# Kernel optimization log

Hardware: AMD Instinct MI355X
Metric: run time of the kernel (lower is better)

Reference implementation:

```python
import jax, jax.numpy as jnp
import numpy as np

N_NODES = 100000


def setup_inputs() -> dict:
    key = jax.random.key(0)
    k_x, k_r, k_c, k_v, k_t = jax.random.split(key, 5)
    n_edges = 3200000
    fin, fout = 512, 128
    x = jax.random.normal(k_x, (N_NODES, fin), dtype=jnp.float32)
    rows = jax.random.randint(k_r, (n_edges,), 0, N_NODES, dtype=jnp.int32)
    cols = jax.random.randint(k_c, (n_edges,), 0, N_NODES, dtype=jnp.int32)
    vals = jax.random.uniform(k_v, (n_edges,), dtype=jnp.float32)
    theta = jax.random.normal(k_t, (fin, fout), dtype=jnp.float32) * (1.0 / np.sqrt(fin))
    bias = jnp.zeros((fout,), dtype=jnp.float32)
    return {"x": x, "rows": rows, "cols": cols, "vals": vals, "theta": theta, "bias": bias}


def reference(x, rows, cols, vals, theta, bias):
    # SpMM: mx[i] = sum over edges (i <- j) of A[i,j] * x[j]
    gathered = vals[:, None] * x[cols]                      # [E, fin]
    mx = jax.ops.segment_sum(gathered, rows, num_segments=N_NODES)  # [N, fin]
    # Dense feature transform + bias + relu
    o = jnp.einsum('nf,fo->no', mx, theta) + bias           # [N, fout]
    return jax.nn.relu(o)
```

## Files before the change

kernel.cpp:

```cpp
#include <hip/hip_runtime.h>
#include <stdint.h>
#include <stddef.h>

#define FIN 512
#define FOUT 128
#define BROWS 160
#define NBK 625
#define SORT_CAP 7680
#define TILE 8192
#define MAXNT 512

typedef __attribute__((ext_vector_type(8))) short short8;
typedef __attribute__((ext_vector_type(4))) float f32x4;

__device__ __forceinline__ unsigned short f2bf(float f) {
  unsigned u = __builtin_bit_cast(unsigned, f);
  u = (u + 0x7fffu + ((u >> 16) & 1u)) >> 16;
  return (unsigned short)u;
}
__device__ __forceinline__ float bf2f(unsigned short h) {
  unsigned u = ((unsigned)h) << 16;
  return __builtin_bit_cast(float, u);
}

__global__ void prep_theta_k(const float* __restrict__ theta,
                             unsigned short* __restrict__ thetaT) {
  int idx = blockIdx.x * blockDim.x + threadIdx.x;
  int n = idx >> 9;
  int k = idx & 511;
  thetaT[idx] = f2bf(theta[k * FOUT + n]);
}

__global__ __launch_bounds__(256) void gemm_k(const float* __restrict__ x,
                                              const unsigned short* __restrict__ thetaT,
                                              unsigned short* __restrict__ yb, int M) {
  __shared__ __align__(16) unsigned short lA[128 * 40];
  __shared__ __align__(16) unsigned short lB[128 * 40];
  const int tid = threadIdx.x;
  const int row0 = blockIdx.x * 128;
  const int wave = tid >> 6, lane = tid & 63;
  const int wm = wave >> 1, wn = wave & 1;
  const int fr = lane & 15, fq = lane >> 4;
  const int arow = tid >> 1, ahalf = tid & 1;

  f32x4 acc[4][4] = {};

  const int grow = row0 + arow;
  const bool aval = (grow < M);
  const float* asrc = x + (size_t)(aval ? grow : 0) * FIN + ahalf * 16;
  const unsigned short* bsrc = thetaT + (size_t)arow * FIN + ahalf * 16;

  for (int k0 = 0; k0 < FIN; k0 += 32) {
    float av[16];
    if (aval) {
      const float4* p = (const float4*)(asrc + k0);
      float4 v0 = p[0], v1 = p[1], v2 = p[2], v3 = p[3];
      av[0] = v0.x; av[1] = v0.y; av[2] = v0.z; av[3] = v0.w;
      av[4] = v1.x; av[5] = v1.y; av[6] = v1.z; av[7] = v1.w;
      av[8] = v2.x; av[9] = v2.y; av[10] = v2.z; av[11] = v2.w;
      av[12] = v3.x; av[13] = v3.y; av[14] = v3.z; av[15] = v3.w;
    } else {
      for (int i = 0; i < 16; i++) av[i] = 0.f;
    }
    unsigned ap[8];
    for (int i = 0; i < 8; i++)
      ap[i] = (unsigned)f2bf(av[2 * i]) | ((unsigned)f2bf(av[2 * i + 1]) << 16);
    uint4* aw = (uint4*)&lA[arow * 40 + ahalf * 16];
    aw[0] = make_uint4(ap[0], ap[1], ap[2], ap[3]);
    aw[1] = make_uint4(ap[4], ap[5], ap[6], ap[7]);

    const uint4* bp = (const uint4*)(bsrc + k0);
    uint4 b0 = bp[0], b1 = bp[1];
    uint4* bw = (uint4*)&lB[arow * 40 + ahalf * 16];
    bw[0] = b0; bw[1] = b1;

    __syncthreads();

    short8 af[4], bfv[4];
#pragma unroll
    for (int m = 0; m < 4; m++)
      af[m] = *(const short8*)&lA[(wm * 64 + m * 16 + fr) * 40 + fq * 8];
#pragma unroll
    for (int n = 0; n < 4; n++)
      bfv[n] = *(const short8*)&lB[(wn * 64 + n * 16 + fr) * 40 + fq * 8];
#pragma unroll
    for (int m = 0; m < 4; m++)
#pragma unroll
      for (int n = 0; n < 4; n++)
        acc[m][n] = __builtin_amdgcn_mfma_f32_16x16x32_bf16(af[m], bfv[n], acc[m][n], 0, 0, 0);

    __syncthreads();
  }

#pragma unroll
  for (int m = 0; m < 4; m++) {
    int rbase = row0 + wm * 64 + m * 16 + fq * 4;
#pragma unroll
    for (int j = 0; j < 4; j++) {
      int r = rbase + j;
      if (r < M) {
        unsigned short* dst = yb + (size_t)r * FOUT + wn * 64;
#pragma unroll
        for (int n = 0; n < 4; n++) dst[n * 16 + fr] = f2bf(acc[m][n][j]);
      }
    }
  }
}

__global__ __launch_bounds__(256) void tilesort_k(const int* __restrict__ rows,
                                                  const int* __restrict__ cols,
                                                  const float* __restrict__ vals,
                                                  unsigned* __restrict__ rec4tile,
                                                  unsigned char* __restrict__ rlotile,
                                                  int* __restrict__ lofs,
                                                  int* __restrict__ btotals, int E) {
  __shared__ int hist[NBK];
  __shared__ int wsum[4];
  __shared__ unsigned srec[TILE];
  __shared__ unsigned char srlo[TILE];
  const int c = blockIdx.x, t = threadIdx.x;
  const int base = c * TILE;
  const int n = (E - base < TILE) ? (E - base) : TILE;

  for (int i = t; i < NBK; i += 256) hist[i] = 0;
  __syncthreads();

#pragma unroll
  for (int k = 0; k < TILE / 256; k++) {
    int i = base + k * 256 + t;
    if (i < E) atomicAdd(&hist[rows[i] / BROWS], 1);
  }
  __syncthreads();

  int c0 = t * 3, c1 = c0 + 1, c2 = c0 + 2;
  int h0 = (c0 < NBK) ? hist[c0] : 0;
  int h1 = (c1 < NBK) ? hist[c1] : 0;
  int h2 = (c2 < NBK) ? hist[c2] : 0;
  if (h0) atomicAdd(&btotals[c0], h0);
  if (h1) atomicAdd(&btotals[c1], h1);
  if (h2) atomicAdd(&btotals[c2], h2);
  int loc = h0 + h1 + h2;
  int lane = t & 63, wv = t >> 6;
  int inc = loc;
  for (int off = 1; off < 64; off <<= 1) {
    int u = __shfl_up(inc, off, 64);
    if (lane >= off) inc += u;
  }
  if (lane == 63) wsum[wv] = inc;
  __syncthreads();
  int excl = inc - loc;
  for (int i = 0; i < 4; i++)
    if (i < wv) excl += wsum[i];

  size_t lbase = (size_t)c * (NBK + 1);
  int e = excl;
  if (c0 <= NBK) lofs[lbase + c0] = e;
  __syncthreads();
  if (c0 < NBK) hist[c0] = e;
  e += h0;
  if (c1 <= NBK) lofs[lbase + c1] = e;
  if (c1 < NBK) hist[c1] = e;
  e += h1;
  if (c2 <= NBK) lofs[lbase + c2] = e;
  if (c2 < NBK) hist[c2] = e;
  __syncthreads();

#pragma unroll
  for (int k = 0; k < TILE / 256; k++) {
    int i = base + k * 256 + t;
    if (i < E) {
      int r = rows[i];
      int b = r / BROWS;
      int p = atomicAdd(&hist[b], 1);
      srec[p] = ((unsigned)cols[i] << 15) | ((unsigned)f2bf(vals[i]) & 0x7fffu);
      srlo[p] = (unsigned char)(r - b * BROWS);
    }
  }
  __syncthreads();

  for (int j = t; j < n; j += 256) {
    rec4tile[base + j] = srec[j];
    rlotile[base + j] = srlo[j];
  }
}

__global__ __launch_bounds__(1024) void bscan_k(const int* __restrict__ btotals,
                                                int* __restrict__ boff,
                                                int* __restrict__ offsets,
                                                int E, int M) {
  __shared__ int tmp[1024];
  int t = threadIdx.x;
  tmp[t] = (t < NBK) ? btotals[t] : 0;
  __syncthreads();
  for (int off = 1; off < 1024; off <<= 1) {
    int v = (t >= off) ? tmp[t - off] : 0;
    __syncthreads();
    tmp[t] += v;
    __syncthreads();
  }
  if (t < NBK) boff[t] = t ? tmp[t - 1] : 0;
  if (t == 0) {
    boff[NBK] = E;
    offsets[M] = E;
  }
}

__global__ __launch_bounds__(256) void bsort_k(const int* __restrict__ boff,
                                               const int* __restrict__ lofs,
                                               const unsigned* __restrict__ rec4tile,
                                               const unsigned char* __restrict__ rlotile,
                                               unsigned* __restrict__ rec4s,
                                               int* __restrict__ offsets,
                                               int NT, int M) {
  __shared__ unsigned s4[SORT_CAP];
  __shared__ unsigned char k8[SORT_CAP];
  __shared__ int lh[256];
  __shared__ int lsc[256];
  __shared__ int wsum[4];
  __shared__ int fsrc[MAXNT];
  __shared__ int fdst[MAXNT];
  __shared__ int flen[MAXNT];
  int b = blockIdx.x, t = threadIdx.x;
  int start = boff[b];

  int ca = 2 * t, cb = 2 * t + 1;
  int la = 0, fa = 0, lb2 = 0, fb = 0;
  if (ca < NT) {
    size_t p = (size_t)ca * (NBK + 1) + b;
    la = lofs[p];
    fa = lofs[p + 1] - la;
  }
  if (cb < NT) {
    size_t p = (size_t)cb * (NBK + 1) + b;
    lb2 = lofs[p];
    fb = lofs[p + 1] - lb2;
  }
  int loc = fa + fb;
  int lane = t & 63, wv = t >> 6;
  int inc = loc;
  for (int off = 1; off < 64; off <<= 1) {
    int u = __shfl_up(inc, off, 64);
    if (lane >= off) inc += u;
  }
  if (lane == 63) wsum[wv] = inc;
  __syncthreads();
  int excl = inc - loc;
  for (int i = 0; i < 4; i++)
    if (i < wv) excl += wsum[i];

  if (ca < NT) {
    fsrc[ca] = ca * TILE + la;
    fdst[ca] = excl;
    flen[ca] = fa;
  }
  if (cb < NT) {
    fsrc[cb] = cb * TILE + lb2;
    fdst[cb] = excl + fa;
    flen[cb] = fb;
  }
  lh[t] = 0;
  __syncthreads();

  int grp = t >> 4, l16 = t & 15;
  for (int f = grp; f < NT; f += 16) {
    int L = flen[f];
    int sd = fdst[f];
    int ss = fsrc[f];
    for (int j = l16; j < L; j += 16) {
      int d = sd + j;
      if (d < SORT_CAP) {
        s4[d] = rec4tile[ss + j];
        k8[d] = rlotile[ss + j];
      }
    }
  }

  int n = boff[b + 1] - start;
  if (n > SORT_CAP) n = SORT_CAP;
  __syncthreads();

  for (int i = t; i < n; i += 256) atomicAdd(&lh[k8[i]], 1);
  __syncthreads();
  lsc[t] = lh[t];
  __syncthreads();
  for (int off = 1; off < 256; off <<= 1) {
    int v = (t >= off) ? lsc[t - off] : 0;
    __syncthreads();
    lsc[t] += v;
    __syncthreads();
  }
  int ex = t ? lsc[t - 1] : 0;
  int row = b * BROWS + t;
  if (t < BROWS && row < M) offsets[row] = start + ex;
  lh[t] = ex;
  __syncthreads();
  for (int i = t; i < n; i += 256) {
    unsigned r = s4[i];
    int p = atomicAdd(&lh[k8[i]], 1);
    rec4s[start + p] = r;
  }
}

__global__ __launch_bounds__(256) void rowv2_k(const int* __restrict__ offsets,
                                               const unsigned* __restrict__ rec4,
                                               const unsigned short* __restrict__ yb,
                                               const float* __restrict__ bias,
                                               float* __restrict__ out, int M) {
  int gid = blockIdx.x * blockDim.x + threadIdx.x;
  int r = gid >> 4;
  int l = gid & 15;
  if (r >= M) return;
  int s = offsets[r], e = offsets[r + 1];
  const unsigned short* src = yb + l * 8;

  float a0 = 0.f, a1 = 0.f, a2 = 0.f, a3 = 0.f, a4 = 0.f, a5 = 0.f, a6 = 0.f, a7 = 0.f;
  float c0 = 0.f, c1 = 0.f, c2 = 0.f, c3 = 0.f, c4 = 0.f, c5 = 0.f, c6 = 0.f, c7 = 0.f;

  int i = s;
  for (; i + 2 <= e; i += 2) {
    unsigned q0 = rec4[i];
    unsigned q1 = rec4[i + 1];
    const uint4 u0 = *(const uint4*)(src + (size_t)(q0 >> 15) * FOUT);
    const uint4 u1 = *(const uint4*)(src + (size_t)(q1 >> 15) * FOUT);
    float v0 = __builtin_bit_cast(float, (q0 & 0x7fffu) << 16);
    float v1 = __builtin_bit_cast(float, (q1 & 0x7fffu) << 16);
    a0 += v0 * __builtin_bit_cast(float, u0.x << 16);
    a1 += v0 * __builtin_bit_cast(float, u0.x & 0xffff0000u);
    a2 += v0 * __builtin_bit_cast(float, u0.y << 16);
    a3 += v0 * __builtin_bit_cast(float, u0.y & 0xffff0000u);
    a4 += v0 * __builtin_bit_cast(float, u0.z << 16);
    a5 += v0 * __builtin_bit_cast(float, u0.z & 0xffff0000u);
    a6 += v0 * __builtin_bit_cast(float, u0.w << 16);
    a7 += v0 * __builtin_bit_cast(float, u0.w & 0xffff0000u);
    c0 += v1 * __builtin_bit_cast(float, u1.x << 16);
    c1 += v1 * __builtin_bit_cast(float, u1.x & 0xffff0000u);
    c2 += v1 * __builtin_bit_cast(float, u1.y << 16);
    c3 += v1 * __builtin_bit_cast(float, u1.y & 0xffff0000u);
    c4 += v1 * __builtin_bit_cast(float, u1.z << 16);
    c5 += v1 * __builtin_bit_cast(float, u1.z & 0xffff0000u);
    c6 += v1 * __builtin_bit_cast(float, u1.w << 16);
    c7 += v1 * __builtin_bit_cast(float, u1.w & 0xffff0000u);
  }
  if (i < e) {
    unsigned q0 = rec4[i];
    const uint4 u0 = *(const uint4*)(src + (size_t)(q0 >> 15) * FOUT);
    float v0 = __builtin_bit_cast(float, (q0 & 0x7fffu) << 16);
    a0 += v0 * __builtin_bit_cast(float, u0.x << 16);
    a1 += v0 * __builtin_bit_cast(float, u0.x & 0xffff0000u);
    a2 += v0 * __builtin_bit_cast(float, u0.y << 16);
    a3 += v0 * __builtin_bit_cast(float, u0.y & 0xffff0000u);
    a4 += v0 * __builtin_bit_cast(float, u0.z << 16);
    a5 += v0 * __builtin_bit_cast(float, u0.z & 0xffff0000u);
    a6 += v0 * __builtin_bit_cast(float, u0.w << 16);
    a7 += v0 * __builtin_bit_cast(float, u0.w & 0xffff0000u);
  }

  const float4 b0 = *(const float4*)(bias + l * 8);
  const float4 b1 = *(const float4*)(bias + l * 8 + 4);
  float* dst = out + (size_t)r * FOUT + l * 8;
  float4 o0, o1;
  o0.x = fmaxf(a0 + c0 + b0.x, 0.f);
  o0.y = fmaxf(a1 + c1 + b0.y, 0.f);
  o0.z = fmaxf(a2 + c2 + b0.z, 0.f);
  o0.w = fmaxf(a3 + c3 + b0.w, 0.f);
  o1.x = fmaxf(a4 + c4 + b1.x, 0.f);
  o1.y = fmaxf(a5 + c5 + b1.y, 0.f);
  o1.z = fmaxf(a6 + c6 + b1.z, 0.f);
  o1.w = fmaxf(a7 + c7 + b1.w, 0.f);
  *(float4*)(dst) = o0;
  *(float4*)(dst + 4) = o1;
}

extern "C" void kernel_launch(void* const* d_in, const int* in_sizes, int n_in,
                              void* d_out, int out_size, void* d_ws, size_t ws_size,
                              hipStream_t stream) {
  const float* x = (const float*)d_in[0];
  const int* rows = (const int*)d_in[1];
  const int* cols = (const int*)d_in[2];
  const float* vals = (const float*)d_in[3];
  const float* theta = (const float*)d_in[4];
  const float* bias = (const float*)d_in[5];
  float* out = (float*)d_out;
  const int M = in_sizes[0] / FIN;
  const int E = in_sizes[1];
  const int NT = (E + TILE - 1) / TILE;

  char* w = (char*)d_ws;
  auto alloc = [&](size_t bytes) {
    char* p = w;
    w += (bytes + 255) & ~(size_t)255;
    return p;
  };
  unsigned short* yb = (unsigned short*)alloc((size_t)M * FOUT * 2);
  unsigned short* thetaT = (unsigned short*)alloc((size_t)FIN * FOUT * 2);
  unsigned* rec4tile = (unsigned*)alloc((size_t)NT * TILE * 4);
  unsigned char* rlotile = (unsigned char*)alloc((size_t)NT * TILE);
  int* lofs = (int*)alloc((size_t)NT * (NBK + 1) * 4);
  int* btotals = (int*)alloc((size_t)NBK * 4);
  int* boff = (int*)alloc((size_t)(NBK + 1) * 4);
  int* offsets = (int*)alloc((size_t)(M + 1) * 4);
  unsigned* rec4s = (unsigned*)alloc((size_t)E * 4);

  hipMemsetAsync(btotals, 0, (size_t)NBK * 4, stream);
  prep_theta_k<<<(FIN * FOUT) / 256, 256, 0, stream>>>(theta, thetaT);
  gemm_k<<<(M + 127) / 128, 256, 0, stream>>>(x, thetaT, yb, M);
  tilesort_k<<<NT, 256, 0, stream>>>(rows, cols, vals, rec4tile, rlotile, lofs, btotals, E);
  bscan_k<<<1, 1024, 0, stream>>>(btotals, boff, offsets, E, M);
  bsort_k<<<NBK, 256, 0, stream>>>(boff, lofs, rec4tile, rlotile, rec4s, offsets, NT, M);
  rowv2_k<<<(M * 16 + 255) / 256, 256, 0, stream>>>(offsets, rec4s, yb, bias, out, M);
}
```

Measured before the change: 294.9 us.

## Split projected features into column planes with XCD-affine persistent gather

The GEMM output is stored as 8 column planes of 16 bf16 each instead of row-major rows. The gather kernel becomes persistent: each block reads its XCD id, works through planes starting from its own, and takes row tiles from per-plane atomic queues. It stages each tile's edge records in LDS. The aim is for each XCD's L2 to hold one small feature plane (about 3.2 MB), so random gathers hit cache. The cost is that every edge record is read 8 times, plus queue atomics and extra barriers.

```diff
diff --git a/kernel.cpp b/kernel.cpp
--- a/kernel.cpp
+++ b/kernel.cpp
@@ -9,6 +9,9 @@
 #define SORT_CAP 7680
 #define TILE 8192
 #define MAXNT 512
+#define NCH 8
+#define PTILE 128
+#define PSTCAP 5120
 
 typedef __attribute__((ext_vector_type(8))) short short8;
 typedef __attribute__((ext_vector_type(4))) float f32x4;
@@ -33,7 +36,7 @@
 
 __global__ __launch_bounds__(256) void gemm_k(const float* __restrict__ x,
                                               const unsigned short* __restrict__ thetaT,
-                                              unsigned short* __restrict__ yb, int M) {
+                                              unsigned short* __restrict__ ybc, int M) {
   __shared__ __align__(16) unsigned short lA[128 * 40];
   __shared__ __align__(16) unsigned short lB[128 * 40];
   const int tid = threadIdx.x;
@@ -99,9 +102,11 @@
     for (int j = 0; j < 4; j++) {
       int r = rbase + j;
       if (r < M) {
-        unsigned short* dst = yb + (size_t)r * FOUT + wn * 64;
-#pragma unroll
-        for (int n = 0; n < 4; n++) dst[n * 16 + fr] = f2bf(acc[m][n][j]);
+#pragma unroll
+        for (int n = 0; n < 4; n++) {
+          int c = wn * 4 + n;
+          ybc[((size_t)c * M + r) * 16 + fr] = f2bf(acc[m][n][j]);
+        }
       }
     }
   }
@@ -187,6 +192,7 @@
 __global__ __launch_bounds__(1024) void bscan_k(const int* __restrict__ btotals,
                                                 int* __restrict__ boff,
                                                 int* __restrict__ offsets,
+                                                int* __restrict__ q,
                                                 int E, int M) {
   __shared__ int tmp[1024];
   int t = threadIdx.x;
@@ -199,6 +205,7 @@
     __syncthreads();
   }
   if (t < NBK) boff[t] = t ? tmp[t - 1] : 0;
+  if (t < NCH) q[t] = 0;
   if (t == 0) {
     boff[NBK] = E;
     offsets[M] = E;
@@ -301,74 +308,130 @@
   }
 }
 
-__global__ __launch_bounds__(256) void rowv2_k(const int* __restrict__ offsets,
-                                               const unsigned* __restrict__ rec4,
-                                               const unsigned short* __restrict__ yb,
-                                               const float* __restrict__ bias,
-                                               float* __restrict__ out, int M) {
-  int gid = blockIdx.x * blockDim.x + threadIdx.x;
-  int r = gid >> 4;
-  int l = gid & 15;
-  if (r >= M) return;
-  int s = offsets[r], e = offsets[r + 1];
-  const unsigned short* src = yb + l * 8;
-
-  float a0 = 0.f, a1 = 0.f, a2 = 0.f, a3 = 0.f, a4 = 0.f, a5 = 0.f, a6 = 0.f, a7 = 0.f;
-  float c0 = 0.f, c1 = 0.f, c2 = 0.f, c3 = 0.f, c4 = 0.f, c5 = 0.f, c6 = 0.f, c7 = 0.f;
-
-  int i = s;
-  for (; i + 2 <= e; i += 2) {
-    unsigned q0 = rec4[i];
-    unsigned q1 = rec4[i + 1];
-    const uint4 u0 = *(const uint4*)(src + (size_t)(q0 >> 15) * FOUT);
-    const uint4 u1 = *(const uint4*)(src + (size_t)(q1 >> 15) * FOUT);
-    float v0 = __builtin_bit_cast(float, (q0 & 0x7fffu) << 16);
-    float v1 = __builtin_bit_cast(float, (q1 & 0x7fffu) << 16);
-    a0 += v0 * __builtin_bit_cast(float, u0.x << 16);
-    a1 += v0 * __builtin_bit_cast(float, u0.x & 0xffff0000u);
-    a2 += v0 * __builtin_bit_cast(float, u0.y << 16);
-    a3 += v0 * __builtin_bit_cast(float, u0.y & 0xffff0000u);
-    a4 += v0 * __builtin_bit_cast(float, u0.z << 16);
-    a5 += v0 * __builtin_bit_cast(float, u0.z & 0xffff0000u);
-    a6 += v0 * __builtin_bit_cast(float, u0.w << 16);
-    a7 += v0 * __builtin_bit_cast(float, u0.w & 0xffff0000u);
-    c0 += v1 * __builtin_bit_cast(float, u1.x << 16);
-    c1 += v1 * __builtin_bit_cast(float, u1.x & 0xffff0000u);
-    c2 += v1 * __builtin_bit_cast(float, u1.y << 16);
-    c3 += v1 * __builtin_bit_cast(float, u1.y & 0xffff0000u);
-    c4 += v1 * __builtin_bit_cast(float, u1.z << 16);
-    c5 += v1 * __builtin_bit_cast(float, u1.z & 0xffff0000u);
-    c6 += v1 * __builtin_bit_cast(float, u1.w << 16);
-    c7 += v1 * __builtin_bit_cast(float, u1.w & 0xffff0000u);
-  }
-  if (i < e) {
-    unsigned q0 = rec4[i];
-    const uint4 u0 = *(const uint4*)(src + (size_t)(q0 >> 15) * FOUT);
-    float v0 = __builtin_bit_cast(float, (q0 & 0x7fffu) << 16);
-    a0 += v0 * __builtin_bit_cast(float, u0.x << 16);
-    a1 += v0 * __builtin_bit_cast(float, u0.x & 0xffff0000u);
-    a2 += v0 * __builtin_bit_cast(float, u0.y << 16);
-    a3 += v0 * __builtin_bit_cast(float, u0.y & 0xffff0000u);
-    a4 += v0 * __builtin_bit_cast(float, u0.z << 16);
-    a5 += v0 * __builtin_bit_cast(float, u0.z & 0xffff0000u);
-    a6 += v0 * __builtin_bit_cast(float, u0.w << 16);
-    a7 += v0 * __builtin_bit_cast(float, u0.w & 0xffff0000u);
-  }
-
-  const float4 b0 = *(const float4*)(bias + l * 8);
-  const float4 b1 = *(const float4*)(bias + l * 8 + 4);
-  float* dst = out + (size_t)r * FOUT + l * 8;
-  float4 o0, o1;
-  o0.x = fmaxf(a0 + c0 + b0.x, 0.f);
-  o0.y = fmaxf(a1 + c1 + b0.y, 0.f);
-  o0.z = fmaxf(a2 + c2 + b0.z, 0.f);
-  o0.w = fmaxf(a3 + c3 + b0.w, 0.f);
-  o1.x = fmaxf(a4 + c4 + b1.x, 0.f);
-  o1.y = fmaxf(a5 + c5 + b1.y, 0.f);
-  o1.z = fmaxf(a6 + c6 + b1.z, 0.f);
-  o1.w = fmaxf(a7 + c7 + b1.w, 0.f);
-  *(float4*)(dst) = o0;
-  *(float4*)(dst + 4) = o1;
+__global__ __launch_bounds__(256) void rowp_k(const int* __restrict__ offsets,
+                                              const unsigned* __restrict__ rec4,
+                                              const unsigned short* __restrict__ ybc,
+                                              const float* __restrict__ bias,
+                                              float* __restrict__ out,
+                                              int* __restrict__ q, int M) {
+  __shared__ unsigned st[PSTCAP];
+  __shared__ int loff[PTILE + 1];
+  __shared__ int s_tile;
+  unsigned xcd = __builtin_amdgcn_s_getreg((31u << 11) | 20u) & 7u;
+  const int ntiles = (M + PTILE - 1) / PTILE;
+  const int t = threadIdx.x;
+  const int rg = t >> 1;
+  const int h = t & 1;
+
+#pragma unroll 1
+  for (int d = 0; d < NCH; d++) {
+    int p = (xcd + d) & 7;
+    const unsigned short* plane = ybc + (size_t)p * M * 16;
+    const float4 bb0 = *(const float4*)(bias + p * 16 + h * 8);
+    const float4 bb1 = *(const float4*)(bias + p * 16 + h * 8 + 4);
+
+#pragma unroll 1
+    while (true) {
+      if (t == 0) s_tile = atomicAdd(&q[p], 1);
+      __syncthreads();
+      int tile = s_tile;
+      __syncthreads();
+      if (tile >= ntiles) break;
+
+      int base = tile * PTILE;
+      if (t <= PTILE) {
+        int idx = base + t;
+        loff[t] = offsets[idx > M ? M : idx];
+      }
+      __syncthreads();
+      int s0 = loff[0];
+      int n = loff[PTILE] - s0;
+      bool fits = (n <= PSTCAP);
+      if (fits) {
+        for (int i = t; i < n; i += 256)
+          st[i] = __builtin_nontemporal_load(&rec4[s0 + i]);
+      }
+      __syncthreads();
+
+      int r = base + rg;
+      if (r < M) {
+        int i0 = loff[rg] - s0, i1 = loff[rg + 1] - s0;
+        float a0 = 0.f, a1 = 0.f, a2 = 0.f, a3 = 0.f;
+        float a4 = 0.f, a5 = 0.f, a6 = 0.f, a7 = 0.f;
+        float c0 = 0.f, c1 = 0.f, c2 = 0.f, c3 = 0.f;
+        float c4 = 0.f, c5 = 0.f, c6 = 0.f, c7 = 0.f;
+        const unsigned short* src = plane + h * 8;
+        if (fits) {
+          int i = i0;
+          for (; i + 2 <= i1; i += 2) {
+            unsigned q0 = st[i];
+            unsigned q1 = st[i + 1];
+            const uint4 u0 = *(const uint4*)(src + (size_t)(q0 >> 15) * 16);
+            const uint4 u1 = *(const uint4*)(src + (size_t)(q1 >> 15) * 16);
+            float v0 = __builtin_bit_cast(float, (q0 & 0x7fffu) << 16);
+            float v1 = __builtin_bit_cast(float, (q1 & 0x7fffu) << 16);
+            a0 += v0 * __builtin_bit_cast(float, u0.x << 16);
+            a1 += v0 * __builtin_bit_cast(float, u0.x & 0xffff0000u);
+            a2 += v0 * __builtin_bit_cast(float, u0.y << 16);
+            a3 += v0 * __builtin_bit_cast(float, u0.y & 0xffff0000u);
+            a4 += v0 * __builtin_bit_cast(float, u0.z << 16);
+            a5 += v0 * __builtin_bit_cast(float, u0.z & 0xffff0000u);
+            a6 += v0 * __builtin_bit_cast(float, u0.w << 16);
+            a7 += v0 * __builtin_bit_cast(float, u0.w & 0xffff0000u);
+            c0 += v1 * __builtin_bit_cast(float, u1.x << 16);
+            c1 += v1 * __builtin_bit_cast(float, u1.x & 0xffff0000u);
+            c2 += v1 * __builtin_bit_cast(float, u1.y << 16);
+            c3 += v1 * __builtin_bit_cast(float, u1.y & 0xffff0000u);
+            c4 += v1 * __builtin_bit_cast(float, u1.z << 16);
+            c5 += v1 * __builtin_bit_cast(float, u1.z & 0xffff0000u);
+            c6 += v1 * __builtin_bit_cast(float, u1.w << 16);
+            c7 += v1 * __builtin_bit_cast(float, u1.w & 0xffff0000u);
+          }
+          if (i < i1) {
+            unsigned q0 = st[i];
+            const uint4 u0 = *(const uint4*)(src + (size_t)(q0 >> 15) * 16);
+            float v0 = __builtin_bit_cast(float, (q0 & 0x7fffu) << 16);
+            a0 += v0 * __builtin_bit_cast(float, u0.x << 16);
+            a1 += v0 * __builtin_bit_cast(float, u0.x & 0xffff0000u);
+            a2 += v0 * __builtin_bit_cast(float, u0.y << 16);
+            a3 += v0 * __builtin_bit_cast(float, u0.y & 0xffff0000u);
+            a4 += v0 * __builtin_bit_cast(float, u0.z << 16);
+            a5 += v0 * __builtin_bit_cast(float, u0.z & 0xffff0000u);
+            a6 += v0 * __builtin_bit_cast(float, u0.w << 16);
+            a7 += v0 * __builtin_bit_cast(float, u0.w & 0xffff0000u);
+          }
+        } else {
+          for (int i = i0; i < i1; i++) {
+            unsigned q0 = rec4[s0 + i];
+            const uint4 u0 = *(const uint4*)(src + (size_t)(q0 >> 15) * 16);
+            float v0 = __builtin_bit_cast(float, (q0 & 0x7fffu) << 16);
+            a0 += v0 * __builtin_bit_cast(float, u0.x << 16);
+            a1 += v0 * __builtin_bit_cast(float, u0.x & 0xffff0000u);
+            a2 += v0 * __builtin_bit_cast(float, u0.y << 16);
+            a3 += v0 * __builtin_bit_cast(float, u0.y & 0xffff0000u);
+            a4 += v0 * __builtin_bit_cast(float, u0.z << 16);
+            a5 += v0 * __builtin_bit_cast(float, u0.z & 0xffff0000u);
+            a6 += v0 * __builtin_bit_cast(float, u0.w << 16);
+            a7 += v0 * __builtin_bit_cast(float, u0.w & 0xffff0000u);
+          }
+        }
+
+        float* dst = out + (size_t)r * FOUT + p * 16 + h * 8;
+        f32x4 o0, o1;
+        o0[0] = fmaxf(a0 + c0 + bb0.x, 0.f);
+        o0[1] = fmaxf(a1 + c1 + bb0.y, 0.f);
+        o0[2] = fmaxf(a2 + c2 + bb0.z, 0.f);
+        o0[3] = fmaxf(a3 + c3 + bb0.w, 0.f);
+        o1[0] = fmaxf(a4 + c4 + bb1.x, 0.f);
+        o1[1] = fmaxf(a5 + c5 + bb1.y, 0.f);
+        o1[2] = fmaxf(a6 + c6 + bb1.z, 0.f);
+        o1[3] = fmaxf(a7 + c7 + bb1.w, 0.f);
+        __builtin_nontemporal_store(o0, (f32x4*)dst);
+        __builtin_nontemporal_store(o1, (f32x4*)(dst + 4));
+      }
+      __syncthreads();
+    }
+  }
 }
 
 extern "C" void kernel_launch(void* const* d_in, const int* in_sizes, int n_in,
@@ -391,7 +454,7 @@
     w += (bytes + 255) & ~(size_t)255;
     return p;
   };
-  unsigned short* yb = (unsigned short*)alloc((size_t)M * FOUT * 2);
+  unsigned short* ybc = (unsigned short*)alloc((size_t)M * FOUT * 2);
   unsigned short* thetaT = (unsigned short*)alloc((size_t)FIN * FOUT * 2);
   unsigned* rec4tile = (unsigned*)alloc((size_t)NT * TILE * 4);
   unsigned char* rlotile = (unsigned char*)alloc((size_t)NT * TILE);
@@ -400,12 +463,13 @@
   int* boff = (int*)alloc((size_t)(NBK + 1) * 4);
   int* offsets = (int*)alloc((size_t)(M + 1) * 4);
   unsigned* rec4s = (unsigned*)alloc((size_t)E * 4);
+  int* q = (int*)alloc((size_t)NCH * 4);
 
   hipMemsetAsync(btotals, 0, (size_t)NBK * 4, stream);
   prep_theta_k<<<(FIN * FOUT) / 256, 256, 0, stream>>>(theta, thetaT);
-  gemm_k<<<(M + 127) / 128, 256, 0, stream>>>(x, thetaT, yb, M);
+  gemm_k<<<(M + 127) / 128, 256, 0, stream>>>(x, thetaT, ybc, M);
   tilesort_k<<<NT, 256, 0, stream>>>(rows, cols, vals, rec4tile, rlotile, lofs, btotals, E);
-  bscan_k<<<1, 1024, 0, stream>>>(btotals, boff, offsets, E, M);
+  bscan_k<<<1, 1024, 0, stream>>>(btotals, boff, offsets, q, E, M);
   bsort_k<<<NBK, 256, 0, stream>>>(boff, lofs, rec4tile, rlotile, rec4s, offsets, NT, M);
-  rowv2_k<<<(M * 16 + 255) / 256, 256, 0, stream>>>(offsets, rec4s, yb, bias, out, M);
-}
+  rowp_k<<<2048, 256, 0, stream>>>(offsets, rec4s, ybc, bias, out, q, M);
+}
```

Result: slower. 499.9 us (+69.5%).
